# Performance work log

Measured on AMD Instinct MI355X. Metric: run time of the kernel, lower is better.

Reference implementation:

```python
import jax, jax.numpy as jnp
import numpy as np

D = 64      # dModel
L = 8       # layers
H = 8       # heads
DK = D // H # head dim
B = 256
SK = 4      # max power-of-two skip AddNorms per layer (log2(L)+1)
EPS = 1e-3  # keras LayerNormalization default


def _ln(x, g, b):
    m = jnp.mean(x, axis=-1, keepdims=True)
    v = jnp.var(x, axis=-1, keepdims=True)
    return (x - m) * jax.lax.rsqrt(v + EPS) * g + b


def _mha(x, wqkv, bqkv, wo, bo):
    # x: [B,S,D]; wqkv: [3,D,H,DK]
    q = jnp.einsum('bsd,dhk->bshk', x, wqkv[0]) + bqkv[0]
    k = jnp.einsum('bsd,dhk->bshk', x, wqkv[1]) + bqkv[1]
    v = jnp.einsum('bsd,dhk->bshk', x, wqkv[2]) + bqkv[2]
    a = jax.nn.softmax(jnp.einsum('bqhk,bshk->bhqs', q, k) * (1.0 / np.float32(np.sqrt(DK))), axis=-1)
    o = jnp.einsum('bhqs,bshk->bqhk', a, v)
    return jnp.einsum('bqhk,hkd->bqd', o, wo) + bo


def _ff(x, w):
    # EinsumDense 'abc,de->ade': sum input over (b,c), outer-multiply by kernel [64,D]
    s = jnp.sum(x, axis=(1, 2))                       # [B]
    h = jax.nn.relu(s[:, None, None] * w[0])          # [B,64,D]
    return jnp.sum(h, axis=(1, 2))[:, None, None] * w[1]


def _gru(xs, h0, k, r, b):
    # keras GRU, reset_after=True; gate order z, r, h; bias [2, 3U]
    bi, br = b[0], b[1]
    def step(h, xt):
        xg = xt @ k + bi
        hg = h @ r + br
        xz, xr, xh = jnp.split(xg, 3, axis=-1)
        hz, hr, hh = jnp.split(hg, 3, axis=-1)
        z = jax.nn.sigmoid(xz + hz)
        rt = jax.nn.sigmoid(xr + hr)
        c = jnp.tanh(xh + rt * hh)
        hn = z * h + (1.0 - z) * c
        return hn, hn
    hT, ys = jax.lax.scan(step, h0, jnp.swapaxes(xs, 0, 1))
    return jnp.swapaxes(ys, 0, 1), hT


def _conv(x, w, b):
    y = jax.lax.conv_general_dilated(x, w, (1, 1, 1), 'VALID',
                                     dimension_numbers=('NDHWC', 'DHWIO', 'NDHWC'))
    return y + b


def _forward(x, state, conv_w4, conv_w3, conv_w2, conv_w1, conv_b, qkv_w, qkv_b,
             out_w, out_b, ff_w, an_g, an_b, gru_k, gru_r, gru_b, skip_g, skip_b):
    Bn = x.shape[0]
    xr = x.reshape(Bn, 64, D + 2 * L)
    last = xr[..., :D]                                            # [B,64,D]
    st_in = jnp.swapaxes(xr[..., D:], 1, 2).reshape(Bn, 2 * L * 64)
    mstate = (state + st_in).reshape(Bn, L, 2, 64)
    bypass, states = [], []
    for i in range(L):
        x4 = last.reshape(Bn, 4, 4, 4, D)
        c4 = _conv(x4, conv_w4[i], conv_b[i, 0]).reshape(Bn, 1, D)
        c3 = _conv(x4, conv_w3[i], conv_b[i, 1]).reshape(Bn, 8, D)
        c2 = _conv(x4, conv_w2[i], conv_b[i, 2]).reshape(Bn, 27, D)
        c1 = _conv(x4, conv_w1[i], conv_b[i, 3]).reshape(Bn, 64, D)
        cc = jnp.concatenate([c4, c3, c2, c1], axis=1)            # [B,100,D]
        a0 = _mha(cc, qkv_w[i, 0], qkv_b[i, 0], out_w[i, 0], out_b[i, 0])
        d0 = _ln(_ff(a0, ff_w[i, 0]) + last, an_g[i, 0], an_b[i, 0])  # dropout = id
        gp = jnp.swapaxes(d0, 1, 2)                               # [B,D,64]
        fore, fs = _gru(gp, mstate[:, i, 0], gru_k[i, 0], gru_r[i, 0], gru_b[i, 0])
        back, bs = _gru(gp[:, ::-1], mstate[:, i, 1], gru_k[i, 1], gru_r[i, 1], gru_b[i, 1])
        states.append(jnp.stack([fs, bs], axis=1))                # [B,2,64]
        ap = jnp.swapaxes(jnp.concatenate([fore, back], axis=2), 1, 2)  # [B,128,D]
        a1 = _mha(ap, qkv_w[i, 1], qkv_b[i, 1], out_w[i, 1], out_b[i, 1])
        d1 = _ln(_ff(a1, ff_w[i, 1]) + d0, an_g[i, 1], an_b[i, 1])
        bypass.append(d1)
        last = d1
        j, s = 1, 0
        while (i + 1) % j == 0:
            last = _ln(bypass[i - j + 1] + last, skip_g[i, s], skip_b[i, s])
            j *= 2
            s += 1
    st = jnp.stack(states, axis=1)                                # [B,L,2,64]
    out_state = st.reshape(Bn, L * 2 * 64)
    out_sd = jnp.swapaxes(st.reshape(Bn, 2 * L, 64), 1, 2)        # [B,64,2L]
    out = jnp.concatenate([last, out_sd], axis=2).reshape(Bn, 64 * (D + 2 * L))
    return out, out_state


def setup_inputs() -> dict:
    key = jax.random.key(0)
    ks = jax.random.split(key, 20)
    r = lambda k, s, sc: sc * jax.random.normal(k, s, dtype=jnp.float32)
    return {
        'x': r(ks[0], (B, 64 * (D + 2 * L)), 1.0),
        'state': r(ks[1], (B, 2 * L * 64), 1.0),
        'conv_w4': r(ks[2], (L, 4, 4, 4, D, D), 0.05),
        'conv_w3': r(ks[3], (L, 3, 3, 3, D, D), 0.05),
        'conv_w2': r(ks[4], (L, 2, 2, 2, D, D), 0.05),
        'conv_w1': r(ks[5], (L, 1, 1, 1, D, D), 0.05),
        'conv_b': r(ks[6], (L, 4, D), 0.02),
        'qkv_w': r(ks[7], (L, 2, 3, D, H, DK), 0.1),
        'qkv_b': r(ks[8], (L, 2, 3, H, DK), 0.02),
        'out_w': r(ks[9], (L, 2, H, DK, D), 0.1),
        'out_b': r(ks[10], (L, 2, D), 0.02),
        'ff_w': r(ks[11], (L, 2, 2, 64, D), 0.02),
        'an_g': 1.0 + r(ks[12], (L, 2, D), 0.02),
        'an_b': r(ks[13], (L, 2, D), 0.02),
        'gru_k': r(ks[14], (L, 2, 64, 3 * 64), 0.1),
        'gru_r': r(ks[15], (L, 2, 64, 3 * 64), 0.1),
        'gru_b': r(ks[16], (L, 2, 2, 3 * 64), 0.02),
        'skip_g': 1.0 + r(ks[17], (L, SK, D), 0.02),
        'skip_b': r(ks[18], (L, SK, D), 0.02),
    }


def reference(x, state, conv_w4, conv_w3, conv_w2, conv_w1, conv_b, qkv_w, qkv_b,
              out_w, out_b, ff_w, an_g, an_b, gru_k, gru_r, gru_b, skip_g, skip_b):
    return _forward(x, state, conv_w4, conv_w3, conv_w2, conv_w1, conv_b, qkv_w,
                    qkv_b, out_w, out_b, ff_w, an_g, an_b, gru_k, gru_r, gru_b,
                    skip_g, skip_b)
```

## Files before the change

kernel.cpp:

```cpp
#include <hip/hip_runtime.h>
#include <hip/hip_bf16.h>


#define TPB 512

constexpr int O_LAST = 0;
constexpr int O_D0T  = 4096;
constexpr int O_BIG  = 8448;
constexpr int O_MST  = 17152;
constexpr int O_RED  = 18176;
constexpr int AR     = 18304;
constexpr int SMF    = 40832;

constexpr int WST  = AR;
constexpr int QKH  = AR + 4096;
constexpr int RINV = AR + 20480;
constexpr int CSUM = AR + 21504;
constexpr int C4P  = AR + 20480;
constexpr int XG   = AR;
constexpr int GHB  = AR + 12288;

constexpr int WOS  = O_RED;
constexpr int BOS  = O_RED + 64;
constexpr int ACCS = O_RED + 65;
constexpr int HSW  = O_RED + 66;
constexpr int HSV  = O_RED + 74;

__device__ __forceinline__ float b2f(unsigned s){ return __builtin_bit_cast(float, s<<16); }

template<int BF> __device__ __forceinline__ float ldf(const void* p, long i){
  if (BF){ unsigned v = ((unsigned)((const unsigned short*)p)[i]) << 16;
           return __builtin_bit_cast(float, v); }
  return ((const float*)p)[i];
}
template<int BF> __device__ __forceinline__ void ldw4(const void* p, long i,
                                                      float&a,float&b,float&c,float&d){
  if (BF){ uint2 u = *(const uint2*)((const unsigned short*)p + i);
    a=b2f(u.x&0xffffu); b=b2f(u.x>>16); c=b2f(u.y&0xffffu); d=b2f(u.y>>16);
  } else { float4 f = *(const float4*)((const float*)p + i); a=f.x;b=f.y;c=f.z;d=f.w; }
}
template<int BF> __device__ __forceinline__ float4 ld4v(const void* p, long i){
  float4 r; ldw4<BF>(p, i, r.x, r.y, r.z, r.w); return r;
}
template<int BF> __device__ __forceinline__ void ld8(const void* p, long i, float* v){
  if (BF){
    uint4 u = *(const uint4*)((const unsigned short*)p + i);
    v[0]=b2f(u.x&0xffffu); v[1]=b2f(u.x>>16);
    v[2]=b2f(u.y&0xffffu); v[3]=b2f(u.y>>16);
    v[4]=b2f(u.z&0xffffu); v[5]=b2f(u.z>>16);
    v[6]=b2f(u.w&0xffffu); v[7]=b2f(u.w>>16);
  } else {
    float4 a=*(const float4*)((const float*)p+i), b=*(const float4*)((const float*)p+i+4);
    v[0]=a.x;v[1]=a.y;v[2]=a.z;v[3]=a.w;v[4]=b.x;v[5]=b.y;v[6]=b.z;v[7]=b.w;
  }
}
template<int BF> __device__ __forceinline__ void stf(void* p, long i, float v){
  if (BF){ unsigned u=__builtin_bit_cast(unsigned,v);
           u += 0x7FFFu + ((u>>16)&1u);
           ((unsigned short*)p)[i]=(unsigned short)(u>>16); }
  else ((float*)p)[i]=v;
}
__device__ __forceinline__ float dot8(float4 a0, float4 a1, float4 b0, float4 b1){
  return a0.x*b0.x+a0.y*b0.y+a0.z*b0.z+a0.w*b0.w
       + a1.x*b1.x+a1.y*b1.y+a1.z*b1.z+a1.w*b1.w;
}
__device__ __forceinline__ void fma4(float* a, float s, float4 w){
  a[0]+=s*w.x; a[1]+=s*w.y; a[2]+=s*w.z; a[3]+=s*w.w;
}
template<int BF> __device__ __forceinline__ void stage4k(float* sm, int dst,
                                                         const void* w, long base){
  int e0 = threadIdx.x * 8;
  float v[8]; ld8<BF>(w, base + e0, v);
  float* dp = sm + dst + e0;
  *(float4*)dp     = make_float4(v[0],v[1],v[2],v[3]);
  *(float4*)(dp+4) = make_float4(v[4],v[5],v[6],v[7]);
}

template<int BF> __device__ void mha_ff_ln(float* sm, int li, int jj, int S,
    const void* qw, const void* qb, const void* ow, const void* ob,
    const void* ffw, const void* ang, const void* anb, const void* cbp, int do_c4)
{
  const int tid = threadIdx.x;
  const int b2  = li*2 + jj;
  const float SC = 0.35355339059327378f;
  const int S8 = S*8;

  stage4k<BF>(sm, WST, qw, (long)(b2*3+0)*4096);
  if (tid < 64){
    float s = 0; long wb = ((long)b2*64 + tid)*64;
    for (int d=0; d<64; d+=4){ float a,b,c,e; ldw4<BF>(ow, wb+d, a,b,c,e); s += a+b+c+e; }
    sm[WOS+tid] = s;
  } else if (tid == 64){
    float s = 0; long bb = (long)b2*64;
    for (int d=0; d<64; ++d) s += ldf<BF>(ob, bb+d);
    sm[BOS] = s;
  } else if (do_c4 && tid >= 448){
    int n = tid - 448;
    float a = ldf<BF>(cbp, (long)(li*4+0)*64 + n);
    #pragma unroll
    for (int rt=0; rt<8; ++rt) a += sm[C4P + rt*64 + n];
    sm[O_BIG + n] = a;
  }
  __syncthreads();

  const int ntile = (S>>2)*16;
  #pragma unroll 1
  for (int m=0; m<2; ++m){
    if (m==1){
      __syncthreads();
      stage4k<BF>(sm, WST, qw, (long)(b2*3+1)*4096);
      __syncthreads();
    }
    if (tid < ntile){
      int pt = tid>>4, nt = tid&15, s0 = pt*4, n0 = nt*4;
      float bias[4]; ldw4<BF>(qb, (long)(b2*3+m)*64 + n0, bias[0],bias[1],bias[2],bias[3]);
      float acc[4][4];
      #pragma unroll
      for (int pp=0;pp<4;++pp){ acc[pp][0]=bias[0]; acc[pp][1]=bias[1]; acc[pp][2]=bias[2]; acc[pp][3]=bias[3]; }
      const float* Wb = sm + WST + n0;
      #pragma unroll 2
      for (int k0=0; k0<64; k0+=4){
        float4 w0 = *(const float4*)(Wb + (k0+0)*64);
        float4 w1 = *(const float4*)(Wb + (k0+1)*64);
        float4 w2 = *(const float4*)(Wb + (k0+2)*64);
        float4 w3 = *(const float4*)(Wb + (k0+3)*64);
        #pragma unroll
        for (int pp=0; pp<4; ++pp){
          float4 xv = *(const float4*)(sm + O_BIG + (s0+pp)*68 + k0);
          fma4(acc[pp], xv.x, w0); fma4(acc[pp], xv.y, w1);
          fma4(acc[pp], xv.z, w2); fma4(acc[pp], xv.w, w3);
        }
      }
      int h = n0>>3, c0 = n0&7;
      #pragma unroll
      for (int pp=0; pp<4; ++pp)
        *(float4*)(sm + QKH + m*8192 + h*S8 + (s0+pp)*8 + c0) =
          make_float4(acc[pp][0],acc[pp][1],acc[pp][2],acc[pp][3]);
    }
  }
  __syncthreads();

  { int h = tid>>6, l = tid&63;
    const float* Qb = sm + QKH + h*S8;
    const float* Kb = sm + QKH + 8192 + h*S8;
    float4 qa0 = *(const float4*)(Qb + l*8), qa1 = *(const float4*)(Qb + l*8 + 4);
    bool v2 = (l+64) < S;
    float4 qb0 = make_float4(0,0,0,0), qb1 = qb0;
    if (v2){ qb0 = *(const float4*)(Qb + (l+64)*8); qb1 = *(const float4*)(Qb + (l+64)*8 + 4); }
    float s1 = 0.f, s2 = 0.f;
    for (int s=0; s<S; ++s){
      float4 k0 = *(const float4*)(Kb + s*8), k1 = *(const float4*)(Kb + s*8 + 4);
      s1 += __expf(dot8(qa0,qa1,k0,k1)*SC);
      if (v2) s2 += __expf(dot8(qb0,qb1,k0,k1)*SC);
    }
    sm[RINV + h*S + l] = 1.f/s1;
    if (v2) sm[RINV + h*S + l+64] = 1.f/s2;
  }
  __syncthreads();

  { int h = tid>>6, l = tid&63;
    const float* Qb = sm + QKH + h*S8;
    const float* Kb = sm + QKH + 8192 + h*S8;
    float4 ka0 = *(const float4*)(Kb + l*8), ka1 = *(const float4*)(Kb + l*8 + 4);
    bool v2 = (l+64) < S;
    float4 kb0 = make_float4(0,0,0,0), kb1 = kb0;
    if (v2){ kb0 = *(const float4*)(Kb + (l+64)*8); kb1 = *(const float4*)(Kb + (l+64)*8 + 4); }
    float c1 = 0.f, c2 = 0.f;
    for (int q=0; q<S; ++q){
      float4 q0 = *(const float4*)(Qb + q*8), q1 = *(const float4*)(Qb + q*8 + 4);
      float ri = sm[RINV + h*S + q];
      c1 += __expf(dot8(q0,q1,ka0,ka1)*SC)*ri;
      if (v2) c2 += __expf(dot8(q0,q1,kb0,kb1)*SC)*ri;
    }
    sm[CSUM + h*S + l] = c1;
    if (v2) sm[CSUM + h*S + l+64] = c2;
  }
  __syncthreads();

  { int h = tid>>6, d = tid&63;
    float a = 0.f;
    for (int s=0; s<S; ++s) a += sm[CSUM + h*S + s]*sm[O_BIG + s*68 + d];
    sm[RINV + h*65 + d] = a;
    stage4k<BF>(sm, WST, qw, (long)(b2*3+2)*4096);
  }
  __syncthreads();

  if (tid < 64){
    int h = tid>>3;
    float a = 0.f;
    #pragma unroll 8
    for (int d=0; d<64; ++d) a += sm[RINV + h*65 + d]*sm[WST + d*64 + tid];
    a += (float)S*ldf<BF>(qb, (long)(b2*3+2)*64 + tid);
    float part = a*sm[WOS + tid];
    part += __shfl_xor(part,32); part += __shfl_xor(part,16); part += __shfl_xor(part,8);
    part += __shfl_xor(part,4);  part += __shfl_xor(part,2);  part += __shfl_xor(part,1);
    if (tid == 0) sm[ACCS] = part + (float)S*sm[BOS];
  }
  __syncthreads();
  const float s_scalar = sm[ACCS];

  float part = 0;
  { long fb = (long)(b2*2)*4096;
    for (int q4=tid; q4<1024; q4+=TPB){
      float a0,a1,a2,a3; ldw4<BF>(ffw, fb + (long)q4*4, a0,a1,a2,a3);
      part += fmaxf(s_scalar*a0,0.f)+fmaxf(s_scalar*a1,0.f)
            + fmaxf(s_scalar*a2,0.f)+fmaxf(s_scalar*a3,0.f); } }
  part += __shfl_xor(part,32); part += __shfl_xor(part,16); part += __shfl_xor(part,8);
  part += __shfl_xor(part,4);  part += __shfl_xor(part,2);  part += __shfl_xor(part,1);
  if ((tid&63)==0) sm[HSW + (tid>>6)] = part;
  __syncthreads();
  if (tid == 0){ float v=0; for (int w=0;w<8;++w) v += sm[HSW+w]; sm[HSV]=v; }
  __syncthreads();
  const float hs = sm[HSV];

  { int r = tid>>3, prt = tid&7;
    long f1b = (long)(b2*2+1)*4096 + r*64 + prt*8;
    float rs[8];
    if (jj == 0){
      const float4* R = (const float4*)(sm + O_LAST + r*64 + prt*8);
      float4 r0 = R[0], r1 = R[1];
      rs[0]=r0.x; rs[1]=r0.y; rs[2]=r0.z; rs[3]=r0.w;
      rs[4]=r1.x; rs[5]=r1.y; rs[6]=r1.z; rs[7]=r1.w;
    } else {
      #pragma unroll
      for (int e=0;e<8;++e) rs[e] = sm[O_D0T + (prt*8+e)*68 + r];
    }
    float w[8];
    ldw4<BF>(ffw, f1b,   w[0],w[1],w[2],w[3]);
    ldw4<BF>(ffw, f1b+4, w[4],w[5],w[6],w[7]);
    float f[8]; float s1=0, s2=0;
    #pragma unroll
    for (int e=0;e<8;++e){ float fv = hs*w[e] + rs[e]; f[e]=fv; s1+=fv; s2+=fv*fv; }
    s1 += __shfl_xor(s1,4); s1 += __shfl_xor(s1,2); s1 += __shfl_xor(s1,1);
    s2 += __shfl_xor(s2,4); s2 += __shfl_xor(s2,2); s2 += __shfl_xor(s2,1);
    float mean = s1*0.015625f, var = s2*0.015625f - mean*mean;
    float rstd = rsqrtf(var + 1e-3f);
    long gb2 = (long)b2*64 + prt*8;
    float g[8], bbv[8];
    ldw4<BF>(ang, gb2,   g[0],g[1],g[2],g[3]);   ldw4<BF>(ang, gb2+4, g[4],g[5],g[6],g[7]);
    ldw4<BF>(anb, gb2,   bbv[0],bbv[1],bbv[2],bbv[3]); ldw4<BF>(anb, gb2+4, bbv[4],bbv[5],bbv[6],bbv[7]);
    if (jj == 0){
      #pragma unroll
      for (int e=0;e<8;++e) sm[O_D0T + (prt*8+e)*68 + r] = (f[e]-mean)*rstd*g[e] + bbv[e];
    } else {
      float* dst = sm + O_LAST + r*64 + prt*8;
      #pragma unroll
      for (int e=0;e<8;++e) dst[e] = (f[e]-mean)*rstd*g[e] + bbv[e];
    }
  }
  __syncthreads();
}

__device__ __forceinline__ float gru_cell(float xz, float xr, float xh,
                                          float az, float ar, float hh, float hmy){
  float z  = 1.f/(1.f + __expf(-az));
  float rt = 1.f/(1.f + __expf(-ar));
  float ca = xh + rt*hh; ca = fminf(fmaxf(ca, -15.f), 15.f);
  float e2 = __expf(2.f*ca);
  float cand = (e2-1.f)/(e2+1.f);
  return z*hmy + (1.f-z)*cand;
}

template<int BF> __device__ void gru_stage(float* sm, int li,
    const void* gk, const void* grr, const void* gbb)
{
  const int tid = threadIdx.x;
  const int dirw = (tid>>6)&1, jl = tid&63;
  float hmy=0, brz=0, brr=0, brh=0, bi=0;
  int hdir = 0, hgg = 0;

  if constexpr (BF){
    unsigned pkz[32], pkr[32], pkh[32];
    unsigned kpk[32];
    const unsigned short* G  = (const unsigned short*)grr;
    const unsigned short* GK = (const unsigned short*)gk;
    if (tid < 128){
      long rb = (long)((li*2+dirw)*64)*192;
      #pragma unroll
      for (int q2=0; q2<32; ++q2){
        long i0 = rb + (long)(2*q2)*192 + jl, i1 = rb + (long)(2*q2+1)*192 + jl;
        pkz[q2] = (unsigned)G[i0]     | ((unsigned)G[i1]<<16);
        pkr[q2] = (unsigned)G[i0+64]  | ((unsigned)G[i1+64]<<16);
        pkh[q2] = (unsigned)G[i0+128] | ((unsigned)G[i1+128]<<16);
      }
      long bb = (long)((li*2+dirw)*2+1)*192;
      brz = ldf<BF>(gbb, bb+jl); brr = ldf<BF>(gbb, bb+64+jl); brh = ldf<BF>(gbb, bb+128+jl);
      hmy = sm[O_MST + (li*2+dirw)*64 + jl];
      sm[GHB + dirw*64 + jl] = hmy;
    } else {
      int c = tid-128; hdir = (c>=192); hgg = c - hdir*192;
      long kb = (long)((li*2+hdir)*64)*192;
      #pragma unroll
      for (int q2=0; q2<32; ++q2)
        kpk[q2] = (unsigned)GK[kb + (long)(2*q2)*192 + hgg]
                | ((unsigned)GK[kb + (long)(2*q2+1)*192 + hgg]<<16);
      bi = ldf<BF>(gbb, (long)((li*2+hdir)*2)*192 + hgg);
    }
    __syncthreads();
    if (tid >= 128){
      for (int lt=0; lt<16; ++lt){
        int xi = hdir ? (63-lt) : lt;
        const float* XP = sm + O_D0T + xi*68;
        float a = bi;
        #pragma unroll
        for (int k2=0; k2<16; ++k2){
          float4 xv = *(const float4*)(XP + 4*k2);
          unsigned p0 = kpk[2*k2], p1 = kpk[2*k2+1];
          a += xv.x*b2f(p0) + xv.y*b2f(p0>>16) + xv.z*b2f(p1) + xv.w*b2f(p1>>16);
        }
        sm[XG + lt*384 + hdir*192 + hgg] = a;
      }
    }
    __syncthreads();
    for (int it=0; it<4; ++it){
      if (tid < 128){
        const float* HP = sm + GHB + dirw*64;
        for (int lt=0; lt<16; ++lt){
          const float* ring = sm + XG + (it&1)*6144 + lt*384 + dirw*192;
          float xz = ring[jl], xr = ring[64+jl], xh = ring[128+jl];
          float az = brz, ar = brr, hh = brh;
          #pragma unroll
          for (int k2=0; k2<16; ++k2){
            float4 hv = *(const float4*)(HP + 4*k2);
            unsigned z0=pkz[2*k2], z1=pkz[2*k2+1];
            unsigned r0=pkr[2*k2], r1=pkr[2*k2+1];
            unsigned h0=pkh[2*k2], h1=pkh[2*k2+1];
            az += hv.x*b2f(z0) + hv.y*b2f(z0>>16) + hv.z*b2f(z1) + hv.w*b2f(z1>>16);
            ar += hv.x*b2f(r0) + hv.y*b2f(r0>>16) + hv.z*b2f(r1) + hv.w*b2f(r1>>16);
            hh += hv.x*b2f(h0) + hv.y*b2f(h0>>16) + hv.z*b2f(h1) + hv.w*b2f(h1>>16);
          }
          float hn = gru_cell(xz, xr, xh, az+xz*0.f+xz- xz + az*0.f + az - az + az, ar+xr, hh, hmy);
          hn = gru_cell(xz, xr, xh, az+xz, ar+xr, hh, hmy);
          hmy = hn;
          sm[O_BIG + (dirw*64+jl)*68 + (it*16+lt)] = hn;
          sm[GHB + dirw*64 + jl] = hn;
        }
      } else if (it < 3){
        int pre0 = (it+1)*16, buf = (it+1)&1;
        for (int lt=0; lt<16; ++lt){
          int pre = pre0+lt;
          int xi = hdir ? (63-pre) : pre;
          const float* XP = sm + O_D0T + xi*68;
          float a = bi;
          #pragma unroll
          for (int k2=0; k2<16; ++k2){
            float4 xv = *(const float4*)(XP + 4*k2);
            unsigned p0 = kpk[2*k2], p1 = kpk[2*k2+1];
            a += xv.x*b2f(p0) + xv.y*b2f(p0>>16) + xv.z*b2f(p1) + xv.w*b2f(p1>>16);
          }
          sm[XG + buf*6144 + lt*384 + hdir*192 + hgg] = a;
        }
      }
      __syncthreads();
    }
    if (tid < 128) sm[O_MST + (li*2+dirw)*64 + jl] = hmy;
    __syncthreads();
  } else {
    float rza[64], rra[64], rha[64], kc[64];
    if (tid < 128){
      long rb = (long)((li*2+dirw)*64)*192;
      #pragma unroll
      for (int q=0; q<64; ++q){
        rza[q] = ldf<BF>(grr, rb + (long)q*192 +       jl);
        rra[q] = ldf<BF>(grr, rb + (long)q*192 +  64 + jl);
        rha[q] = ldf<BF>(grr, rb + (long)q*192 + 128 + jl);
      }
      long bb = (long)((li*2+dirw)*2+1)*192;
      brz = ldf<BF>(gbb, bb+jl); brr = ldf<BF>(gbb, bb+64+jl); brh = ldf<BF>(gbb, bb+128+jl);
      hmy = sm[O_MST + (li*2+dirw)*64 + jl];
      sm[GHB + dirw*64 + jl] = hmy;
    } else {
      int c = tid-128; hdir = (c>=192); hgg = c - hdir*192;
      long kb = (long)((li*2+hdir)*64)*192;
      #pragma unroll
      for (int q=0; q<64; ++q) kc[q] = ldf<BF>(gk, kb + (long)q*192 + hgg);
      bi = ldf<BF>(gbb, (long)((li*2+hdir)*2)*192 + hgg);
    }
    __syncthreads();
    if (tid >= 128){
      for (int lt=0; lt<16; ++lt){
        int xi = hdir ? (63-lt) : lt;
        const float* XP = sm + O_D0T + xi*68;
        float a = bi;
        #pragma unroll
        for (int k=0;k<16;++k){
          float4 xv = *(const float4*)(XP + 4*k);
          a += xv.x*kc[4*k] + xv.y*kc[4*k+1] + xv.z*kc[4*k+2] + xv.w*kc[4*k+3];
        }
        sm[XG + lt*384 + hdir*192 + hgg] = a;
      }
    }
    __syncthreads();
    for (int it=0; it<4; ++it){
      if (tid < 128){
        const float* HP = sm + GHB + dirw*64;
        for (int lt=0; lt<16; ++lt){
          const float* ring = sm + XG + (it&1)*6144 + lt*384 + dirw*192;
          float xz = ring[jl], xr = ring[64+jl], xh = ring[128+jl];
          float az = brz, ar = brr, hh = brh;
          #pragma unroll
          for (int k=0;k<16;++k){
            float4 hv = *(const float4*)(HP + 4*k);
            az += hv.x*rza[4*k] + hv.y*rza[4*k+1] + hv.z*rza[4*k+2] + hv.w*rza[4*k+3];
            ar += hv.x*rra[4*k] + hv.y*rra[4*k+1] + hv.z*rra[4*k+2] + hv.w*rra[4*k+3];
            hh += hv.x*rha[4*k] + hv.y*rha[4*k+1] + hv.z*rha[4*k+2] + hv.w*rha[4*k+3];
          }
          float hn = gru_cell(xz, xr, xh, az+xz, ar+xr, hh, hmy);
          hmy = hn;
          sm[O_BIG + (dirw*64+jl)*68 + (it*16+lt)] = hn;
          sm[GHB + dirw*64 + jl] = hn;
        }
      } else if (it < 3){
        int pre0 = (it+1)*16, buf = (it+1)&1;
        for (int lt=0; lt<16; ++lt){
          int pre = pre0+lt;
          int xi = hdir ? (63-pre) : pre;
          const float* XP = sm + O_D0T + xi*68;
          float a = bi;
          #pragma unroll
          for (int k=0;k<16;++k){
            float4 xv = *(const float4*)(XP + 4*k);
            a += xv.x*kc[4*k] + xv.y*kc[4*k+1] + xv.z*kc[4*k+2] + xv.w*kc[4*k+3];
          }
          sm[XG + buf*6144 + lt*384 + hdir*192 + hgg] = a;
        }
      }
      __syncthreads();
    }
    if (tid < 128) sm[O_MST + (li*2+dirw)*64 + jl] = hmy;
    __syncthreads();
  }
}

template<int BF> __device__ void run_all(float* sm,
    const void* x, const void* st, const void* cw4, const void* cw3, const void* cw2,
    const void* cw1, const void* cb, const void* qw, const void* qb, const void* ow,
    const void* ob, const void* ffw, const void* ang, const void* anb, const void* gk,
    const void* grr, const void* gbb, const void* sg, const void* sb2,
    void* outp, float* bypass)
{
  const int tid = threadIdx.x;
  const int b   = blockIdx.x;

  for (int o=tid; o<4096; o+=TPB){ int p=o>>6, d=o&63;
    sm[O_LAST+o] = ldf<BF>(x, (long)b*5120 + p*80 + d); }
  for (int o=tid; o<1024; o+=TPB){ int c=o>>6, j=o&63;
    sm[O_MST+o] = ldf<BF>(st, (long)b*1024 + o) + ldf<BF>(x, (long)b*5120 + j*80 + 64 + c); }
  __syncthreads();

  for (int li=0; li<8; ++li){
    if (tid < 128){
      int rt = tid>>4, nt = tid&15, n0 = nt*4;
      float a1[8][4], a4[4] = {0,0,0,0};
      { float c1b[4]; ldw4<BF>(cb, (long)(li*4+3)*64 + n0, c1b[0],c1b[1],c1b[2],c1b[3]);
        #pragma unroll
        for (int rr=0;rr<8;++rr){ a1[rr][0]=c1b[0]; a1[rr][1]=c1b[1]; a1[rr][2]=c1b[2]; a1[rr][3]=c1b[3]; } }
      for (int k0=0; k0<64; k0+=4){
        float4 w1[4];
        #pragma unroll
        for (int kk=0;kk<4;++kk) w1[kk] = ld4v<BF>(cw1, (long)li*4096 + (long)(k0+kk)*64 + n0);
        #pragma unroll
        for (int rr=0; rr<8; ++rr){
          int r = rt*8 + rr;
          float4 xv = *(const float4*)(sm + O_LAST + r*64 + k0);
          fma4(a1[rr], xv.x, w1[0]); fma4(a1[rr], xv.y, w1[1]);
          fma4(a1[rr], xv.z, w1[2]); fma4(a1[rr], xv.w, w1[3]);
          float4 w4a = ld4v<BF>(cw4, (long)(li*64+r)*4096 + (long)(k0+0)*64 + n0);
          float4 w4b = ld4v<BF>(cw4, (long)(li*64+r)*4096 + (long)(k0+1)*64 + n0);
          float4 w4c = ld4v<BF>(cw4, (long)(li*64+r)*4096 + (long)(k0+2)*64 + n0);
          float4 w4d = ld4v<BF>(cw4, (long)(li*64+r)*4096 + (long)(k0+3)*64 + n0);
          fma4(a4, xv.x, w4a); fma4(a4, xv.y, w4b);
          fma4(a4, xv.z, w4c); fma4(a4, xv.w, w4d);
        }
      }
      #pragma unroll
      for (int rr=0; rr<8; ++rr)
        *(float4*)(sm + O_BIG + (36+rt*8+rr)*68 + n0) = make_float4(a1[rr][0],a1[rr][1],a1[rr][2],a1[rr][3]);
      *(float4*)(sm + C4P + rt*64 + n0) = make_float4(a4[0],a4[1],a4[2],a4[3]);
    } else if (tid < 384){
      int t = tid-128, rt2 = t>>4, nt = t&15, n0 = nt*4;
      int r0 = rt2*2;
      if (r0 < 27){
        int nr = (r0+1 < 27) ? 2 : 1;
        float a2[2][4];
        { float bb[4]; ldw4<BF>(cb, (long)(li*4+2)*64 + n0, bb[0],bb[1],bb[2],bb[3]);
          for (int rr=0;rr<2;++rr){ a2[rr][0]=bb[0]; a2[rr][1]=bb[1]; a2[rr][2]=bb[2]; a2[rr][3]=bb[3]; } }
        int ozA[2], oyA[2], oxA[2];
        for (int rr=0; rr<nr; ++rr){
          int r = r0+rr, oz = r/9, rm = r-oz*9, oy = rm/3;
          ozA[rr]=oz; oyA[rr]=oy; oxA[rr]=rm-oy*3;
        }
        for (int kk=0; kk<8; ++kk){
          int kz=(kk>>2)&1, ky=(kk>>1)&1, kx=kk&1;
          int posA[2];
          for (int rr=0; rr<nr; ++rr)
            posA[rr] = (ozA[rr]+kz)*16 + (oyA[rr]+ky)*4 + (oxA[rr]+kx);
          long wb = (long)(li*8+kk)*4096 + n0;
          for (int k0=0; k0<64; k0+=4){
            float4 w0 = ld4v<BF>(cw2, wb + (long)(k0+0)*64);
            float4 w1 = ld4v<BF>(cw2, wb + (long)(k0+1)*64);
            float4 w2 = ld4v<BF>(cw2, wb + (long)(k0+2)*64);
            float4 w3 = ld4v<BF>(cw2, wb + (long)(k0+3)*64);
            for (int rr=0; rr<nr; ++rr){
              float4 xv = *(const float4*)(sm + O_LAST + posA[rr]*64 + k0);
              fma4(a2[rr], xv.x, w0); fma4(a2[rr], xv.y, w1);
              fma4(a2[rr], xv.z, w2); fma4(a2[rr], xv.w, w3);
            }
          }
        }
        for (int rr=0; rr<nr; ++rr)
          *(float4*)(sm + O_BIG + (9+r0+rr)*68 + n0) = make_float4(a2[rr][0],a2[rr][1],a2[rr][2],a2[rr][3]);
      }
    } else {
      int t = tid-384, r3 = t>>4, nt = t&15, n0 = nt*4;
      int oz3=(r3>>2)&1, oy3=(r3>>1)&1, ox3=r3&1;
      float a3[4];
      ldw4<BF>(cb, (long)(li*4+1)*64 + n0, a3[0],a3[1],a3[2],a3[3]);
      for (int kp=0; kp<27; ++kp){
        int kz = kp/9, kr = kp-kz*9, ky = kr/3, kx = kr-ky*3;
        int pos = (oz3+kz)*16 + (oy3+ky)*4 + (ox3+kx);
        long wb = (long)(li*27+kp)*4096 + n0;
        for (int k0=0; k0<64; k0+=4){
          float4 w0 = ld4v<BF>(cw3, wb + (long)(k0+0)*64);
          float4 w1 = ld4v<BF>(cw3, wb + (long)(k0+1)*64);
          float4 w2 = ld4v<BF>(cw3, wb + (long)(k0+2)*64);
          float4 w3 = ld4v<BF>(cw3, wb + (long)(k0+3)*64);
          float4 xv = *(const float4*)(sm + O_LAST + pos*64 + k0);
          fma4(a3, xv.x, w0); fma4(a3, xv.y, w1);
          fma4(a3, xv.z, w2); fma4(a3, xv.w, w3);
        }
      }
      *(float4*)(sm + O_BIG + (1+r3)*68 + n0) = make_float4(a3[0],a3[1],a3[2],a3[3]);
    }
    __syncthreads();

    mha_ff_ln<BF>(sm, li, 0, 100, qw, qb, ow, ob, ffw, ang, anb, cb, 1);

    gru_stage<BF>(sm, li, gk, grr, gbb);

    mha_ff_ln<BF>(sm, li, 1, 128, qw, qb, ow, ob, ffw, ang, anb, cb, 0);

    if ((li&1) == 0){
      float* bp = bypass + ((long)b*4 + (li>>1))*4096;
      for (int o=tid*4; o<4096; o+=TPB*4)
        *(float4*)(bp + o) = *(const float4*)(sm + O_LAST + o);
    }
    __syncthreads();
    { int jmp = 1, sidx = 0;
      while (((li+1) % jmp) == 0){
        int src = li - jmp + 1;
        { int r = tid>>3, prt = tid&7;
          const float4* Lv = (const float4*)(sm + O_LAST + r*64 + prt*8);
          float4 l0 = Lv[0], l1 = Lv[1];
          float Lr[8] = {l0.x,l0.y,l0.z,l0.w,l1.x,l1.y,l1.z,l1.w};
          float av[8];
          if (src == li){
            #pragma unroll
            for (int e=0;e<8;++e) av[e] = Lr[e];
          } else {
            const float4* bpr = (const float4*)(bypass + ((long)b*4 + (src>>1))*4096 + r*64 + prt*8);
            float4 b0 = bpr[0], b1 = bpr[1];
            av[0]=b0.x; av[1]=b0.y; av[2]=b0.z; av[3]=b0.w;
            av[4]=b1.x; av[5]=b1.y; av[6]=b1.z; av[7]=b1.w;
          }
          float f[8]; float s1=0, s2=0;
          #pragma unroll
          for (int e=0; e<8; ++e){ float fv = av[e] + Lr[e]; f[e]=fv; s1+=fv; s2+=fv*fv; }
          s1 += __shfl_xor(s1,4); s1 += __shfl_xor(s1,2); s1 += __shfl_xor(s1,1);
          s2 += __shfl_xor(s2,4); s2 += __shfl_xor(s2,2); s2 += __shfl_xor(s2,1);
          float mean = s1*0.015625f, var = s2*0.015625f - mean*mean;
          float rstd = rsqrtf(var + 1e-3f);
          long gb2 = (long)(li*4 + sidx)*64 + prt*8;
          float g[8], bbv[8];
          ldw4<BF>(sg,  gb2,   g[0],g[1],g[2],g[3]);     ldw4<BF>(sg,  gb2+4, g[4],g[5],g[6],g[7]);
          ldw4<BF>(sb2, gb2,   bbv[0],bbv[1],bbv[2],bbv[3]); ldw4<BF>(sb2, gb2+4, bbv[4],bbv[5],bbv[6],bbv[7]);
          float* W = sm + O_LAST + r*64 + prt*8;
          #pragma unroll
          for (int e=0; e<8; ++e) W[e] = (f[e]-mean)*rstd*g[e] + bbv[e];
        }
        jmp *= 2; ++sidx;
        __syncthreads();
      } }
  }

  for (int o=tid; o<5120; o+=TPB){
    int p = o/80, d = o - p*80;
    float v = (d<64) ? sm[O_LAST + p*64 + d] : sm[O_MST + (d-64)*64 + p];
    stf<BF>(outp, (long)b*5120 + o, v);
  }
  for (int o=tid; o<1024; o+=TPB)
    stf<BF>(outp, (long)256*5120 + (long)b*1024 + o, sm[O_MST+o]);
}

__global__ void detect_dtype(const void* ang, int* flag){
  if (threadIdx.x == 0 && blockIdx.x == 0){
    const unsigned* w = (const unsigned*)ang;
    int good = 0;
    for (int k=0; k<64; ++k){
      unsigned u = w[k];
      float lo = __builtin_bit_cast(float, (u & 0xFFFFu) << 16);
      float hi = __builtin_bit_cast(float, u & 0xFFFF0000u);
      if (lo > 0.7f && lo < 1.4f && hi > 0.7f && hi < 1.4f) ++good;
    }
    *flag = (good >= 48) ? 1 : 0;
  }
}

__global__ void __launch_bounds__(TPB, 1) converter_kernel(
    const void* x, const void* st, const void* cw4, const void* cw3, const void* cw2,
    const void* cw1, const void* cb, const void* qw, const void* qb, const void* ow,
    const void* ob, const void* ffw, const void* ang, const void* anb, const void* gk,
    const void* grr, const void* gbb, const void* sg, const void* sb2,
    const int* flagp, void* outp, float* bypass)
{
  extern __shared__ float sm[];
  if (*flagp)
    run_all<1>(sm, x, st, cw4, cw3, cw2, cw1, cb, qw, qb, ow, ob, ffw, ang, anb,
               gk, grr, gbb, sg, sb2, outp, bypass);
  else
    run_all<0>(sm, x, st, cw4, cw3, cw2, cw1, cb, qw, qb, ow, ob, ffw, ang, anb,
               gk, grr, gbb, sg, sb2, outp, bypass);
}

extern "C" void kernel_launch(void* const* d_in, const int* in_sizes, int n_in,
                              void* d_out, int out_size, void* d_ws, size_t ws_size,
                              hipStream_t stream) {
  (void)in_sizes; (void)n_in; (void)out_size; (void)ws_size;
  int*   flag   = (int*)d_ws;
  float* bypass = (float*)((char*)d_ws + 256);

  hipFuncSetAttribute(reinterpret_cast<const void*>(converter_kernel),
                      hipFuncAttributeMaxDynamicSharedMemorySize, SMF*4);

  detect_dtype<<<1, 64, 0, stream>>>(d_in[12], flag);
  converter_kernel<<<256, TPB, SMF*4, stream>>>(
      d_in[0], d_in[1], d_in[2], d_in[3], d_in[4], d_in[5], d_in[6], d_in[7],
      d_in[8], d_in[9], d_in[10], d_in[11], d_in[12], d_in[13], d_in[14],
      d_in[15], d_in[16], d_in[17], d_in[18], flag, d_out, bypass);
}
```

Baseline: 3.235 ms.

## Stage bf16 GRU recurrent weights in LDS instead of registers, halve XG chunks

In the bf16 GRU path, the recurrent weight matrix is no longer held in 96 packed registers per thread. It is now cooperatively loaded and repacked into shared memory with a padded row stride and read back as uint4. The input-projection ring buffer is shrunk to chunks of 8 timesteps over 8 iterations so that the weights fit in LDS. A redundant duplicate gru_cell call is also removed. The aim is to cut register pressure and scratch spills and drop the wasted cell evaluation, at the cost of extra LDS reads per step and twice as many block barriers.

```diff
diff --git a/kernel.cpp b/kernel.cpp
--- a/kernel.cpp
+++ b/kernel.cpp
@@ -17,8 +17,11 @@
 constexpr int RINV = AR + 20480;
 constexpr int CSUM = AR + 21504;
 constexpr int C4P  = AR + 20480;
-constexpr int XG   = AR;
-constexpr int GHB  = AR + 12288;
+constexpr int GW   = AR;
+constexpr int GHB1 = AR + 12800;
+constexpr int XG1  = AR + 12928;
+constexpr int XG0  = AR;
+constexpr int GHB0 = AR + 12288;
 
 constexpr int WOS  = O_RED;
 constexpr int BOS  = O_RED + 64;
@@ -251,8 +254,7 @@
   __syncthreads();
 }
 
-__device__ __forceinline__ float gru_cell(float xz, float xr, float xh,
-                                          float az, float ar, float hh, float hmy){
+__device__ __forceinline__ float gru_cell(float xh, float az, float ar, float hh, float hmy){
   float z  = 1.f/(1.f + __expf(-az));
   float rt = 1.f/(1.f + __expf(-ar));
   float ca = xh + rt*hh; ca = fminf(fmaxf(ca, -15.f), 15.f);
@@ -270,23 +272,30 @@
   int hdir = 0, hgg = 0;
 
   if constexpr (BF){
-    unsigned pkz[32], pkr[32], pkh[32];
-    unsigned kpk[32];
+    unsigned* smU = (unsigned*)sm;
     const unsigned short* G  = (const unsigned short*)grr;
     const unsigned short* GK = (const unsigned short*)gk;
+    for (int t = tid; t < 3072; t += TPB){
+      int j4 = t & 15, rest = t >> 4;
+      int q2 = rest & 31, rest2 = rest >> 5;
+      int gate = rest2 % 3, dir = rest2 / 3;
+      long src = ((long)((li*2+dir)*64 + 2*q2))*192 + gate*64 + j4*4;
+      unsigned a01 = *(const unsigned*)(G + src);
+      unsigned a23 = *(const unsigned*)(G + src + 2);
+      unsigned b01 = *(const unsigned*)(G + src + 192);
+      unsigned b23 = *(const unsigned*)(G + src + 194);
+      unsigned* dst = smU + GW + (dir*64 + j4*4)*100 + gate*32 + q2;
+      dst[0]   = (a01 & 0xffffu) | (b01 << 16);
+      dst[100] = (a01 >> 16)     | (b01 & 0xffff0000u);
+      dst[200] = (a23 & 0xffffu) | (b23 << 16);
+      dst[300] = (a23 >> 16)     | (b23 & 0xffff0000u);
+    }
+    unsigned kpk[32];
     if (tid < 128){
-      long rb = (long)((li*2+dirw)*64)*192;
-      #pragma unroll
-      for (int q2=0; q2<32; ++q2){
-        long i0 = rb + (long)(2*q2)*192 + jl, i1 = rb + (long)(2*q2+1)*192 + jl;
-        pkz[q2] = (unsigned)G[i0]     | ((unsigned)G[i1]<<16);
-        pkr[q2] = (unsigned)G[i0+64]  | ((unsigned)G[i1+64]<<16);
-        pkh[q2] = (unsigned)G[i0+128] | ((unsigned)G[i1+128]<<16);
-      }
       long bb = (long)((li*2+dirw)*2+1)*192;
       brz = ldf<BF>(gbb, bb+jl); brr = ldf<BF>(gbb, bb+64+jl); brh = ldf<BF>(gbb, bb+128+jl);
       hmy = sm[O_MST + (li*2+dirw)*64 + jl];
-      sm[GHB + dirw*64 + jl] = hmy;
+      sm[GHB1 + dirw*64 + jl] = hmy;
     } else {
       int c = tid-128; hdir = (c>=192); hgg = c - hdir*192;
       long kb = (long)((li*2+hdir)*64)*192;
@@ -298,7 +307,7 @@
     }
     __syncthreads();
     if (tid >= 128){
-      for (int lt=0; lt<16; ++lt){
+      for (int lt=0; lt<8; ++lt){
         int xi = hdir ? (63-lt) : lt;
         const float* XP = sm + O_D0T + xi*68;
         float a = bi;
@@ -308,36 +317,38 @@
           unsigned p0 = kpk[2*k2], p1 = kpk[2*k2+1];
           a += xv.x*b2f(p0) + xv.y*b2f(p0>>16) + xv.z*b2f(p1) + xv.w*b2f(p1>>16);
         }
-        sm[XG + lt*384 + hdir*192 + hgg] = a;
-      }
-    }
-    __syncthreads();
-    for (int it=0; it<4; ++it){
+        sm[XG1 + lt*384 + hdir*192 + hgg] = a;
+      }
+    }
+    __syncthreads();
+    for (int it=0; it<8; ++it){
       if (tid < 128){
-        const float* HP = sm + GHB + dirw*64;
-        for (int lt=0; lt<16; ++lt){
-          const float* ring = sm + XG + (it&1)*6144 + lt*384 + dirw*192;
+        const float* HP = sm + GHB1 + dirw*64;
+        const uint4* Wrow = (const uint4*)(smU + GW + (dirw*64+jl)*100);
+        for (int lt=0; lt<8; ++lt){
+          const float* ring = sm + XG1 + (it&1)*3072 + lt*384 + dirw*192;
           float xz = ring[jl], xr = ring[64+jl], xh = ring[128+jl];
           float az = brz, ar = brr, hh = brh;
           #pragma unroll
-          for (int k2=0; k2<16; ++k2){
-            float4 hv = *(const float4*)(HP + 4*k2);
-            unsigned z0=pkz[2*k2], z1=pkz[2*k2+1];
-            unsigned r0=pkr[2*k2], r1=pkr[2*k2+1];
-            unsigned h0=pkh[2*k2], h1=pkh[2*k2+1];
-            az += hv.x*b2f(z0) + hv.y*b2f(z0>>16) + hv.z*b2f(z1) + hv.w*b2f(z1>>16);
-            ar += hv.x*b2f(r0) + hv.y*b2f(r0>>16) + hv.z*b2f(r1) + hv.w*b2f(r1>>16);
-            hh += hv.x*b2f(h0) + hv.y*b2f(h0>>16) + hv.z*b2f(h1) + hv.w*b2f(h1>>16);
+          for (int k2=0; k2<8; ++k2){
+            float4 h0 = *(const float4*)(HP + 8*k2);
+            float4 h1 = *(const float4*)(HP + 8*k2 + 4);
+            uint4 z = Wrow[k2], r = Wrow[8+k2], h = Wrow[16+k2];
+            az += h0.x*b2f(z.x)+h0.y*b2f(z.x>>16)+h0.z*b2f(z.y)+h0.w*b2f(z.y>>16)
+                + h1.x*b2f(z.z)+h1.y*b2f(z.z>>16)+h1.z*b2f(z.w)+h1.w*b2f(z.w>>16);
+            ar += h0.x*b2f(r.x)+h0.y*b2f(r.x>>16)+h0.z*b2f(r.y)+h0.w*b2f(r.y>>16)
+                + h1.x*b2f(r.z)+h1.y*b2f(r.z>>16)+h1.z*b2f(r.w)+h1.w*b2f(r.w>>16);
+            hh += h0.x*b2f(h.x)+h0.y*b2f(h.x>>16)+h0.z*b2f(h.y)+h0.w*b2f(h.y>>16)
+                + h1.x*b2f(h.z)+h1.y*b2f(h.z>>16)+h1.z*b2f(h.w)+h1.w*b2f(h.w>>16);
           }
-          float hn = gru_cell(xz, xr, xh, az+xz*0.f+xz- xz + az*0.f + az - az + az, ar+xr, hh, hmy);
-          hn = gru_cell(xz, xr, xh, az+xz, ar+xr, hh, hmy);
+          float hn = gru_cell(xh, az+xz, ar+xr, hh, hmy);
           hmy = hn;
-          sm[O_BIG + (dirw*64+jl)*68 + (it*16+lt)] = hn;
-          sm[GHB + dirw*64 + jl] = hn;
-        }
-      } else if (it < 3){
-        int pre0 = (it+1)*16, buf = (it+1)&1;
-        for (int lt=0; lt<16; ++lt){
+          sm[O_BIG + (dirw*64+jl)*68 + (it*8+lt)] = hn;
+          sm[GHB1 + dirw*64 + jl] = hn;
+        }
+      } else if (it < 7){
+        int pre0 = (it+1)*8, buf = (it+1)&1;
+        for (int lt=0; lt<8; ++lt){
           int pre = pre0+lt;
           int xi = hdir ? (63-pre) : pre;
           const float* XP = sm + O_D0T + xi*68;
@@ -348,7 +359,7 @@
             unsigned p0 = kpk[2*k2], p1 = kpk[2*k2+1];
             a += xv.x*b2f(p0) + xv.y*b2f(p0>>16) + xv.z*b2f(p1) + xv.w*b2f(p1>>16);
           }
-          sm[XG + buf*6144 + lt*384 + hdir*192 + hgg] = a;
+          sm[XG1 + buf*3072 + lt*384 + hdir*192 + hgg] = a;
         }
       }
       __syncthreads();
@@ -368,7 +379,7 @@
       long bb = (long)((li*2+dirw)*2+1)*192;
       brz = ldf<BF>(gbb, bb+jl); brr = ldf<BF>(gbb, bb+64+jl); brh = ldf<BF>(gbb, bb+128+jl);
       hmy = sm[O_MST + (li*2+dirw)*64 + jl];
-      sm[GHB + dirw*64 + jl] = hmy;
+      sm[GHB0 + dirw*64 + jl] = hmy;
     } else {
       int c = tid-128; hdir = (c>=192); hgg = c - hdir*192;
       long kb = (long)((li*2+hdir)*64)*192;
@@ -387,15 +398,15 @@
           float4 xv = *(const float4*)(XP + 4*k);
           a += xv.x*kc[4*k] + xv.y*kc[4*k+1] + xv.z*kc[4*k+2] + xv.w*kc[4*k+3];
         }
-        sm[XG + lt*384 + hdir*192 + hgg] = a;
+        sm[XG0 + lt*384 + hdir*192 + hgg] = a;
       }
     }
     __syncthreads();
     for (int it=0; it<4; ++it){
       if (tid < 128){
-        const float* HP = sm + GHB + dirw*64;
+        const float* HP = sm + GHB0 + dirw*64;
         for (int lt=0; lt<16; ++lt){
-          const float* ring = sm + XG + (it&1)*6144 + lt*384 + dirw*192;
+          const float* ring = sm + XG0 + (it&1)*6144 + lt*384 + dirw*192;
           float xz = ring[jl], xr = ring[64+jl], xh = ring[128+jl];
           float az = brz, ar = brr, hh = brh;
           #pragma unroll
@@ -405,10 +416,10 @@
             ar += hv.x*rra[4*k] + hv.y*rra[4*k+1] + hv.z*rra[4*k+2] + hv.w*rra[4*k+3];
             hh += hv.x*rha[4*k] + hv.y*rha[4*k+1] + hv.z*rha[4*k+2] + hv.w*rha[4*k+3];
           }
-          float hn = gru_cell(xz, xr, xh, az+xz, ar+xr, hh, hmy);
+          float hn = gru_cell(xh, az+xz, ar+xr, hh, hmy);
           hmy = hn;
           sm[O_BIG + (dirw*64+jl)*68 + (it*16+lt)] = hn;
-          sm[GHB + dirw*64 + jl] = hn;
+          sm[GHB0 + dirw*64 + jl] = hn;
         }
       } else if (it < 3){
         int pre0 = (it+1)*16, buf = (it+1)&1;
@@ -422,7 +433,7 @@
             float4 xv = *(const float4*)(XP + 4*k);
             a += xv.x*kc[4*k] + xv.y*kc[4*k+1] + xv.z*kc[4*k+2] + xv.w*kc[4*k+3];
           }
-          sm[XG + buf*6144 + lt*384 + hdir*192 + hgg] = a;
+          sm[XG0 + buf*6144 + lt*384 + hdir*192 + hgg] = a;
         }
       }
       __syncthreads();
@@ -535,9 +546,7 @@
     __syncthreads();
 
     mha_ff_ln<BF>(sm, li, 0, 100, qw, qb, ow, ob, ffw, ang, anb, cb, 1);
-
     gru_stage<BF>(sm, li, gk, grr, gbb);
-
     mha_ff_ln<BF>(sm, li, 1, 128, qw, qb, ow, ob, ffw, ang, anb, cb, 0);
 
     if ((li&1) == 0){
```

New measurement: 3.170 ms. -2.0%, faster.
